# Kernel optimization log

Measured on AMD Instinct MI355X. Metric: run time of the kernel, lower is better.

The kernel has to match this reference:

```python
import jax, jax.numpy as jnp
import numpy as np

N_HEADS = 16

def setup_inputs() -> dict:
    key = jax.random.key(0)
    ks = jax.random.split(key, 7)
    B, S, D = 2, 2048, 1024
    sc = 1.0 / np.sqrt(D)
    return {
        "x": jax.random.normal(ks[0], (B, S, D), dtype=jnp.float32),
        "Wq": jax.random.normal(ks[1], (D, D), dtype=jnp.float32) * sc,
        "bq": jax.random.normal(ks[2], (D,), dtype=jnp.float32) * 0.02,
        "Wk": jax.random.normal(ks[3], (D, D), dtype=jnp.float32) * sc,
        "bk": jax.random.normal(ks[4], (D,), dtype=jnp.float32) * 0.02,
        "Wv": jax.random.normal(ks[5], (D, D), dtype=jnp.float32) * sc,
        "bv": jax.random.normal(ks[6], (D,), dtype=jnp.float32) * 0.02,
    }

def reference(x, Wq, bq, Wk, bk, Wv, bv):
    B, S, D = x.shape
    H = N_HEADS
    W = D // H  # head width
    # QKV projections (torch Linear: x @ W^T + b); here weights stored as [D_in, D_out]
    q = x @ Wq + bq
    k = x @ Wk + bk
    v = x @ Wv + bv
    # split last dim into heads -> [B, H, S, W]
    q = q.reshape(B, S, H, W).transpose(0, 2, 1, 3)
    k = k.reshape(B, S, H, W).transpose(0, 2, 1, 3)
    v = v.reshape(B, S, H, W).transpose(0, 2, 1, 3)
    # scaled dot-product attention; full [B,H,S,S] scores as in original
    scores = jnp.einsum("bhqw,bhkw->bhqk", q, k) / jnp.sqrt(jnp.asarray(W, x.dtype))
    probs = jax.nn.softmax(scores, axis=-1)  # dropout is identity in eval mode
    h = jnp.einsum("bhqk,bhkw->bhqw", probs, v)
    # merge heads -> [B, S, D]
    return h.transpose(0, 2, 1, 3).reshape(B, S, D)
```

## Files before the change

### kernel.cpp

```cpp
#include <hip/hip_runtime.h>

typedef _Float16 H16;
typedef _Float16 half8 __attribute__((ext_vector_type(8)));
typedef _Float16 half4 __attribute__((ext_vector_type(4)));
typedef float f32x4 __attribute__((ext_vector_type(4)));

constexpr int Bb = 2, S = 2048, D = 1024, NH = 16, HW = 64;
constexpr int M = Bb * S;

constexpr size_t XH_OFF = 0;
constexpr size_t WT_OFF = XH_OFF + (size_t)M * D * 2;
constexpr size_t Q_OFF  = WT_OFF + 3ull * D * D * 2;
constexpr size_t K_OFF  = Q_OFF + (size_t)M * D * 2;
constexpr size_t VT_OFF = K_OFF + (size_t)M * D * 2;

#define GLOAD_LDS16(g, l)                                        \
  __builtin_amdgcn_global_load_lds(                              \
      (const __attribute__((address_space(1))) void*)(g),        \
      (__attribute__((address_space(3))) void*)(l), 16, 0, 0)

__global__ __launch_bounds__(256) void prep(const float* __restrict__ x,
                                            H16* __restrict__ xh,
                                            const float* __restrict__ w0,
                                            const float* __restrict__ w1,
                                            const float* __restrict__ w2,
                                            H16* __restrict__ wt) {
  __shared__ H16 tile[64][65];
  const int z = blockIdx.z;
  const int t = threadIdx.x;
  if (z == 0) {
    const int bid = blockIdx.y * 16 + blockIdx.x;
#pragma unroll
    for (int r = 0; r < 8; ++r) {
      size_t i = ((size_t)(bid * 8 + r) * 256 + t) * 8;
      float4 a = *(const float4*)(x + i);
      float4 b = *(const float4*)(x + i + 4);
      half8 h = {(H16)a.x, (H16)a.y, (H16)a.z, (H16)a.w,
                 (H16)b.x, (H16)b.y, (H16)b.z, (H16)b.w};
      *(half8*)(xh + i) = h;
    }
  } else {
    const float* w = z == 1 ? w0 : z == 2 ? w1 : w2;
    H16* out = wt + (size_t)(z - 1) * D * D;
    int c = t & 63, r4 = t >> 6;
    int bx = blockIdx.x * 64, by = blockIdx.y * 64;
#pragma unroll 4
    for (int it = 0; it < 16; ++it) {
      int row = it * 4 + r4;
      tile[c][row] = (H16)w[(size_t)(by + row) * D + bx + c];
    }
    __syncthreads();
#pragma unroll 4
    for (int it = 0; it < 16; ++it) {
      int row = it * 4 + r4;
      out[(size_t)(bx + row) * D + by + c] = tile[row][c];
    }
  }
}

__global__ __launch_bounds__(256) void qkv_gemm(
    const H16* __restrict__ xh, const H16* __restrict__ wt,
    const float* __restrict__ bq, const float* __restrict__ bk,
    const float* __restrict__ bv, H16* __restrict__ qo, H16* __restrict__ ko,
    H16* __restrict__ vto) {
  __shared__ __align__(16) H16 As[128 * 64];
  __shared__ __align__(16) H16 Bs[128 * 64];
  const int lin = blockIdx.x + blockIdx.y * 8 + blockIdx.z * 256;
  const int wid = (lin & 7) * 96 + (lin >> 3);
  const int z = wid >> 8;
  const int rem = wid & 255;
  const int bm = (rem >> 3) * 128, bn = (rem & 7) * 128;
  const H16* w = wt + (size_t)z * D * D;
  const float* bias = z == 0 ? bq : z == 1 ? bk : bv;
  const int t = threadIdx.x;
  const int wave = t >> 6, lane = t & 63;
  const int g = lane >> 4, c = lane & 15;
  const int wm = (wave >> 1) * 64, wn = (wave & 1) * 64;

  const int sw0 = (g ^ (c & 7)) * 8;
  const int sw1 = ((4 + g) ^ (c & 7)) * 8;

  f32x4 acc[4][4] = {};

  for (int kk = 0; kk < D; kk += 64) {
#pragma unroll
    for (int rnd = 0; rnd < 4; ++rnd) {
      int cid = rnd * 256 + t;
      int row = cid >> 3, j = cid & 7;
      int k0 = (j ^ (row & 7)) * 8;
      GLOAD_LDS16(&xh[(size_t)(bm + row) * D + kk + k0], &As[cid * 8]);
      GLOAD_LDS16(&w[(size_t)(bn + row) * D + kk + k0], &Bs[cid * 8]);
    }
    __syncthreads();
#pragma unroll
    for (int kc = 0; kc < 2; ++kc) {
      const int ro = kc ? sw1 : sw0;
      half8 af[4], bf[4];
#pragma unroll
      for (int i = 0; i < 4; ++i) {
        af[i] = *(const half8*)&As[(wm + i * 16 + c) * 64 + ro];
        bf[i] = *(const half8*)&Bs[(wn + i * 16 + c) * 64 + ro];
      }
#pragma unroll
      for (int i = 0; i < 4; ++i)
#pragma unroll
        for (int j2 = 0; j2 < 4; ++j2)
          acc[i][j2] = __builtin_amdgcn_mfma_f32_16x16x32_f16(af[i], bf[j2],
                                                              acc[i][j2], 0, 0, 0);
    }
    __syncthreads();
  }

#pragma unroll
  for (int i = 0; i < 4; ++i) {
#pragma unroll
    for (int j = 0; j < 4; ++j) {
      int coln = bn + wn + j * 16 + c;
      float bse = bias[coln];
      int h = coln >> 6, wcol = coln & 63;
      if (z == 2) {
        int row0 = bm + wm + i * 16 + g * 4;
        int bbx = row0 >> 11, s0 = row0 & (S - 1);
        half4 v4 = {(H16)(acc[i][j][0] + bse), (H16)(acc[i][j][1] + bse),
                    (H16)(acc[i][j][2] + bse), (H16)(acc[i][j][3] + bse)};
        *(half4*)&vto[((size_t)(bbx * NH + h) * HW + wcol) * S + s0] = v4;
      } else {
#pragma unroll
        for (int r = 0; r < 4; ++r) {
          int row = bm + wm + i * 16 + g * 4 + r;
          float val = acc[i][j][r] + bse;
          int bbx = row >> 11, s = row & (S - 1);
          size_t bh = (size_t)(bbx * NH + h);
          if (z == 0)
            qo[(bh * S + s) * HW + wcol] = (H16)val;
          else
            ko[(bh * S + s) * HW + wcol] = (H16)val;
        }
      }
    }
  }
}

__global__ __launch_bounds__(512, 4) void attn(const H16* __restrict__ q,
                                               const H16* __restrict__ k,
                                               const H16* __restrict__ vt,
                                               float* __restrict__ out) {
  constexpr int NIT = S / 128;
  __shared__ __align__(16) H16 Ks[2][2][64 * 64];
  __shared__ __align__(16) H16 Vs[2][2][64 * 64];
  __shared__ float lx[4][2][16];

  const int id = blockIdx.x;
  const int xcd = id & 7, slot = id >> 3;
  const int bh = xcd * 4 + (slot >> 4);
  const int qt = slot & 15;

  const int t = threadIdx.x, wave = t >> 6, lane = t & 63;
  const int kg = wave >> 2, w4 = wave & 3;
  const int g = lane >> 4, c = lane & 15;
  const int q0 = qt * 128 + w4 * 32;
  const H16* qp = q + ((size_t)bh * S + q0) * HW;
  const H16* kp = k + ((size_t)bh * S + kg * (S / 2)) * HW;
  const H16* vp = vt + (size_t)bh * HW * S + kg * (S / 2);

  const int tt = t & 255;
  const int sq = tt >> 3, sj = tt & 7;
  const int kkey = ((sq >> 2) & 3) * 8 + ((sq >> 4) & 1) * 4 + (sq & 3);
  const int scol = (sj ^ (sq & 7)) * 8;
  const H16* kga = kp + (size_t)kkey * HW + scol;
  const H16* kgb = kp + (size_t)(32 + kkey) * HW + scol;
  const H16* vga = vp + (size_t)sq * S + scol;
  const H16* vgb = vp + (size_t)(sq + 32) * S + scol;

#define STAGE(bufi, nck)                                                  \
  {                                                                       \
    GLOAD_LDS16(kga + (size_t)(nck) * HW, &Ks[bufi][kg][tt * 8]);         \
    GLOAD_LDS16(kgb + (size_t)(nck) * HW, &Ks[bufi][kg][2048 + tt * 8]);  \
    GLOAD_LDS16(vga + (nck), &Vs[bufi][kg][tt * 8]);                      \
    GLOAD_LDS16(vgb + (nck), &Vs[bufi][kg][2048 + tt * 8]);               \
  }

  const H16 scq = (H16)(0.125f * 1.44269504088896f);
  half8 qb[2][2];
#pragma unroll
  for (int qg = 0; qg < 2; ++qg) {
    qb[qg][0] = *(const half8*)&qp[(qg * 16 + c) * HW + g * 8];
    qb[qg][1] = *(const half8*)&qp[(qg * 16 + c) * HW + 32 + g * 8];
#pragma unroll
    for (int e = 0; e < 8; ++e) {
      qb[qg][0][e] *= scq;
      qb[qg][1][e] *= scq;
    }
  }

  f32x4 o[4][2] = {};
  float l[2] = {0.f, 0.f};

  const int sw0 = (g ^ (c & 7)) * 8;
  const int sw1 = ((4 + g) ^ (c & 7)) * 8;

  STAGE(0, 0);
  int buf = 0;
  for (int it = 0; it < NIT; ++it) {
    __syncthreads();
    if (it + 1 < NIT) STAGE(buf ^ 1, (it + 1) * 64);

    const H16* ks = Ks[buf][kg];
    const H16* vs = Vs[buf][kg];

    f32x4 st[4][2];
#pragma unroll
    for (int kt = 0; kt < 4; ++kt) {
      const H16* kr = &ks[(kt * 16 + c) * 64];
      half8 ka0 = *(const half8*)&kr[sw0];
      half8 ka1 = *(const half8*)&kr[sw1];
#pragma unroll
      for (int qg = 0; qg < 2; ++qg) {
        f32x4 z = {};
        st[kt][qg] =
            __builtin_amdgcn_mfma_f32_16x16x32_f16(ka0, qb[qg][0], z, 0, 0, 0);
        st[kt][qg] = __builtin_amdgcn_mfma_f32_16x16x32_f16(ka1, qb[qg][1],
                                                            st[kt][qg], 0, 0, 0);
      }
    }

    half8 pb[2][2];
#pragma unroll
    for (int qg = 0; qg < 2; ++qg) {
#pragma unroll
      for (int kt = 0; kt < 4; ++kt) {
        float p0 = __builtin_amdgcn_exp2f(st[kt][qg][0]);
        float p1 = __builtin_amdgcn_exp2f(st[kt][qg][1]);
        float p2 = __builtin_amdgcn_exp2f(st[kt][qg][2]);
        float p3 = __builtin_amdgcn_exp2f(st[kt][qg][3]);
        l[qg] += (p0 + p1) + (p2 + p3);
        pb[qg][kt >> 1][(kt & 1) * 4 + 0] = (H16)p0;
        pb[qg][kt >> 1][(kt & 1) * 4 + 1] = (H16)p1;
        pb[qg][kt >> 1][(kt & 1) * 4 + 2] = (H16)p2;
        pb[qg][kt >> 1][(kt & 1) * 4 + 3] = (H16)p3;
      }
    }

#pragma unroll
    for (int wt = 0; wt < 4; ++wt) {
      const H16* vr = &vs[(wt * 16 + c) * 64];
      half8 va0 = *(const half8*)&vr[sw0];
      half8 va1 = *(const half8*)&vr[sw1];
#pragma unroll
      for (int qg = 0; qg < 2; ++qg) {
        o[wt][qg] = __builtin_amdgcn_mfma_f32_16x16x32_f16(va0, pb[qg][0],
                                                           o[wt][qg], 0, 0, 0);
        o[wt][qg] = __builtin_amdgcn_mfma_f32_16x16x32_f16(va1, pb[qg][1],
                                                           o[wt][qg], 0, 0, 0);
      }
    }
    buf ^= 1;
  }
#undef STAGE

#pragma unroll
  for (int qg = 0; qg < 2; ++qg) {
    l[qg] += __shfl_xor(l[qg], 16, 64);
    l[qg] += __shfl_xor(l[qg], 32, 64);
  }

  __syncthreads();

  float* pex = (float*)Ks;
  if (kg == 1) {
    float* dst = pex + w4 * 2048;
#pragma unroll
    for (int wt = 0; wt < 4; ++wt)
#pragma unroll
      for (int qg = 0; qg < 2; ++qg)
        *(f32x4*)&dst[(wt * 2 + qg) * 256 + lane * 4] = o[wt][qg];
    if (g == 0) {
      lx[w4][0][c] = l[0];
      lx[w4][1][c] = l[1];
    }
  }
  __syncthreads();
  if (kg == 0) {
    const float* src = pex + w4 * 2048;
    const int bbx = bh >> 4, h = bh & 15;
#pragma unroll
    for (int qg = 0; qg < 2; ++qg) {
      const float inv = 1.0f / (l[qg] + lx[w4][qg][c]);
      float* orow = out + ((size_t)bbx * S + q0 + qg * 16 + c) * D + h * HW;
#pragma unroll
      for (int wt = 0; wt < 4; ++wt) {
        f32x4 po = *(const f32x4*)&src[(wt * 2 + qg) * 256 + lane * 4];
        float4 v4 = {(o[wt][qg][0] + po[0]) * inv, (o[wt][qg][1] + po[1]) * inv,
                     (o[wt][qg][2] + po[2]) * inv, (o[wt][qg][3] + po[3]) * inv};
        *(float4*)&orow[wt * 16 + g * 4] = v4;
      }
    }
  }
}

extern "C" void kernel_launch(void* const* d_in, const int* in_sizes, int n_in,
                              void* d_out, int out_size, void* d_ws,
                              size_t ws_size, hipStream_t stream) {
  const float* x = (const float*)d_in[0];
  const float* Wq = (const float*)d_in[1];
  const float* bq = (const float*)d_in[2];
  const float* Wk = (const float*)d_in[3];
  const float* bk = (const float*)d_in[4];
  const float* Wv = (const float*)d_in[5];
  const float* bv = (const float*)d_in[6];
  float* out = (float*)d_out;
  char* ws = (char*)d_ws;
  H16* xh = (H16*)(ws + XH_OFF);
  H16* wt = (H16*)(ws + WT_OFF);
  H16* qw = (H16*)(ws + Q_OFF);
  H16* kw = (H16*)(ws + K_OFF);
  H16* vtw = (H16*)(ws + VT_OFF);

  prep<<<dim3(16, 16, 4), 256, 0, stream>>>(x, xh, Wq, Wk, Wv, wt);
  qkv_gemm<<<dim3(8, 32, 3), 256, 0, stream>>>(xh, wt, bq, bk, bv, qw, kw, vtw);
  attn<<<dim3(512), 512, 0, stream>>>(qw, kw, vtw, out);
}
```

Baseline: 166.5 us.

## Double-buffer QKV GEMM LDS tiles and raise wave priority around MFMA blocks

The QKV projection GEMM now keeps two LDS buffers for the A and B tiles. It issues the global-to-LDS loads for the next k-slice before computing on the current one, which removes the trailing barrier and overlaps memory latency with MFMA work. s_setprio(1)/(0) brackets are also added around the MFMA clusters in both the GEMM and the attention kernel, to favour waves that are issuing matrix ops. The cost is doubled LDS use in the GEMM (64KB), which may reduce occupancy.

```diff
diff --git a/kernel.cpp b/kernel.cpp
--- a/kernel.cpp
+++ b/kernel.cpp
@@ -63,8 +63,8 @@
     const float* __restrict__ bq, const float* __restrict__ bk,
     const float* __restrict__ bv, H16* __restrict__ qo, H16* __restrict__ ko,
     H16* __restrict__ vto) {
-  __shared__ __align__(16) H16 As[128 * 64];
-  __shared__ __align__(16) H16 Bs[128 * 64];
+  __shared__ __align__(16) H16 As[2][128 * 64];
+  __shared__ __align__(16) H16 Bs[2][128 * 64];
   const int lin = blockIdx.x + blockIdx.y * 8 + blockIdx.z * 256;
   const int wid = (lin & 7) * 96 + (lin >> 3);
   const int z = wid >> 8;
@@ -77,39 +77,52 @@
   const int g = lane >> 4, c = lane & 15;
   const int wm = (wave >> 1) * 64, wn = (wave & 1) * 64;
 
+  const int srow = t >> 3, sj = t & 7;
+  const int sk0 = (sj ^ (srow & 7)) * 8;
+
+#define QSTAGE(bufi, kkk)                                                   \
+  {                                                                         \
+    _Pragma("unroll") for (int rnd = 0; rnd < 4; ++rnd) {                   \
+      int row = rnd * 32 + srow;                                            \
+      int cid = rnd * 256 + t;                                              \
+      GLOAD_LDS16(&xh[(size_t)(bm + row) * D + (kkk) + sk0],                \
+                  &As[bufi][cid * 8]);                                      \
+      GLOAD_LDS16(&w[(size_t)(bn + row) * D + (kkk) + sk0],                 \
+                  &Bs[bufi][cid * 8]);                                      \
+    }                                                                       \
+  }
+
   const int sw0 = (g ^ (c & 7)) * 8;
   const int sw1 = ((4 + g) ^ (c & 7)) * 8;
 
   f32x4 acc[4][4] = {};
 
+  QSTAGE(0, 0);
+  int buf = 0;
   for (int kk = 0; kk < D; kk += 64) {
-#pragma unroll
-    for (int rnd = 0; rnd < 4; ++rnd) {
-      int cid = rnd * 256 + t;
-      int row = cid >> 3, j = cid & 7;
-      int k0 = (j ^ (row & 7)) * 8;
-      GLOAD_LDS16(&xh[(size_t)(bm + row) * D + kk + k0], &As[cid * 8]);
-      GLOAD_LDS16(&w[(size_t)(bn + row) * D + kk + k0], &Bs[cid * 8]);
-    }
     __syncthreads();
+    if (kk + 64 < D) QSTAGE(buf ^ 1, kk + 64);
 #pragma unroll
     for (int kc = 0; kc < 2; ++kc) {
       const int ro = kc ? sw1 : sw0;
       half8 af[4], bf[4];
 #pragma unroll
       for (int i = 0; i < 4; ++i) {
-        af[i] = *(const half8*)&As[(wm + i * 16 + c) * 64 + ro];
-        bf[i] = *(const half8*)&Bs[(wn + i * 16 + c) * 64 + ro];
-      }
+        af[i] = *(const half8*)&As[buf][(wm + i * 16 + c) * 64 + ro];
+        bf[i] = *(const half8*)&Bs[buf][(wn + i * 16 + c) * 64 + ro];
+      }
+      __builtin_amdgcn_s_setprio(1);
 #pragma unroll
       for (int i = 0; i < 4; ++i)
 #pragma unroll
         for (int j2 = 0; j2 < 4; ++j2)
           acc[i][j2] = __builtin_amdgcn_mfma_f32_16x16x32_f16(af[i], bf[j2],
                                                               acc[i][j2], 0, 0, 0);
-    }
-    __syncthreads();
-  }
+      __builtin_amdgcn_s_setprio(0);
+    }
+    buf ^= 1;
+  }
+#undef QSTAGE
 
 #pragma unroll
   for (int i = 0; i < 4; ++i) {
@@ -214,6 +227,7 @@
       const H16* kr = &ks[(kt * 16 + c) * 64];
       half8 ka0 = *(const half8*)&kr[sw0];
       half8 ka1 = *(const half8*)&kr[sw1];
+      __builtin_amdgcn_s_setprio(1);
 #pragma unroll
       for (int qg = 0; qg < 2; ++qg) {
         f32x4 z = {};
@@ -222,6 +236,7 @@
         st[kt][qg] = __builtin_amdgcn_mfma_f32_16x16x32_f16(ka1, qb[qg][1],
                                                             st[kt][qg], 0, 0, 0);
       }
+      __builtin_amdgcn_s_setprio(0);
     }
 
     half8 pb[2][2];
@@ -246,6 +261,7 @@
       const H16* vr = &vs[(wt * 16 + c) * 64];
       half8 va0 = *(const half8*)&vr[sw0];
       half8 va1 = *(const half8*)&vr[sw1];
+      __builtin_amdgcn_s_setprio(1);
 #pragma unroll
       for (int qg = 0; qg < 2; ++qg) {
         o[wt][qg] = __builtin_amdgcn_mfma_f32_16x16x32_f16(va0, pb[qg][0],
@@ -253,6 +269,7 @@
         o[wt][qg] = __builtin_amdgcn_mfma_f32_16x16x32_f16(va1, pb[qg][1],
                                                            o[wt][qg], 0, 0, 0);
       }
+      __builtin_amdgcn_s_setprio(0);
     }
     buf ^= 1;
   }
```

Result: no change. 169.0 us (+1.5%).

## Load K/V fragments directly from global memory instead of LDS staging

Applied to the files above, without the earlier changes.

Removes the double-buffered LDS staging of K and V tiles (global_load_lds plus __syncthreads per iteration). Each lane now reads its MFMA operand fragments straight from global memory, relying on L1/L2 since the four query waves share the same keys. It also interleaves the QK MFMAs with exp2 per key tile and adds s_setprio around MFMA groups. This drops barriers and LDS traffic but adds redundant global loads, with no software prefetch to hide their latency.

```diff
diff --git a/kernel.cpp b/kernel.cpp
--- a/kernel.cpp
+++ b/kernel.cpp
@@ -146,8 +146,7 @@
                                                const H16* __restrict__ vt,
                                                float* __restrict__ out) {
   constexpr int NIT = S / 128;
-  __shared__ __align__(16) H16 Ks[2][2][64 * 64];
-  __shared__ __align__(16) H16 Vs[2][2][64 * 64];
+  __shared__ float pex[4][2048];
   __shared__ float lx[4][2][16];
 
   const int id = blockIdx.x;
@@ -163,23 +162,6 @@
   const H16* kp = k + ((size_t)bh * S + kg * (S / 2)) * HW;
   const H16* vp = vt + (size_t)bh * HW * S + kg * (S / 2);
 
-  const int tt = t & 255;
-  const int sq = tt >> 3, sj = tt & 7;
-  const int kkey = ((sq >> 2) & 3) * 8 + ((sq >> 4) & 1) * 4 + (sq & 3);
-  const int scol = (sj ^ (sq & 7)) * 8;
-  const H16* kga = kp + (size_t)kkey * HW + scol;
-  const H16* kgb = kp + (size_t)(32 + kkey) * HW + scol;
-  const H16* vga = vp + (size_t)sq * S + scol;
-  const H16* vgb = vp + (size_t)(sq + 32) * S + scol;
-
-#define STAGE(bufi, nck)                                                  \
-  {                                                                       \
-    GLOAD_LDS16(kga + (size_t)(nck) * HW, &Ks[bufi][kg][tt * 8]);         \
-    GLOAD_LDS16(kgb + (size_t)(nck) * HW, &Ks[bufi][kg][2048 + tt * 8]);  \
-    GLOAD_LDS16(vga + (nck), &Vs[bufi][kg][tt * 8]);                      \
-    GLOAD_LDS16(vgb + (nck), &Vs[bufi][kg][2048 + tt * 8]);               \
-  }
-
   const H16 scq = (H16)(0.125f * 1.44269504088896f);
   half8 qb[2][2];
 #pragma unroll
@@ -193,46 +175,44 @@
     }
   }
 
+  const H16* klane = kp + (size_t)(8 * (c >> 2) + (c & 3)) * HW + g * 8;
+  const H16* vlane = vp + (size_t)c * S + g * 8;
+
   f32x4 o[4][2] = {};
   float l[2] = {0.f, 0.f};
 
-  const int sw0 = (g ^ (c & 7)) * 8;
-  const int sw1 = ((4 + g) ^ (c & 7)) * 8;
-
-  STAGE(0, 0);
-  int buf = 0;
   for (int it = 0; it < NIT; ++it) {
-    __syncthreads();
-    if (it + 1 < NIT) STAGE(buf ^ 1, (it + 1) * 64);
-
-    const H16* ks = Ks[buf][kg];
-    const H16* vs = Vs[buf][kg];
-
-    f32x4 st[4][2];
+    const int kofs = it * 64 * HW;
+    const int vofs = it * 64;
+
+    half8 kf[4][2];
 #pragma unroll
     for (int kt = 0; kt < 4; ++kt) {
-      const H16* kr = &ks[(kt * 16 + c) * 64];
-      half8 ka0 = *(const half8*)&kr[sw0];
-      half8 ka1 = *(const half8*)&kr[sw1];
+      const int ko = kofs + (32 * (kt >> 1) + 4 * (kt & 1)) * HW;
+      kf[kt][0] = *(const half8*)(klane + ko);
+      kf[kt][1] = *(const half8*)(klane + ko + 32);
+    }
+
+    half8 pb[2][2];
+#pragma unroll
+    for (int kt = 0; kt < 4; ++kt) {
+      f32x4 st[2];
+      __builtin_amdgcn_s_setprio(1);
 #pragma unroll
       for (int qg = 0; qg < 2; ++qg) {
         f32x4 z = {};
-        st[kt][qg] =
-            __builtin_amdgcn_mfma_f32_16x16x32_f16(ka0, qb[qg][0], z, 0, 0, 0);
-        st[kt][qg] = __builtin_amdgcn_mfma_f32_16x16x32_f16(ka1, qb[qg][1],
-                                                            st[kt][qg], 0, 0, 0);
-      }
-    }
-
-    half8 pb[2][2];
-#pragma unroll
-    for (int qg = 0; qg < 2; ++qg) {
-#pragma unroll
-      for (int kt = 0; kt < 4; ++kt) {
-        float p0 = __builtin_amdgcn_exp2f(st[kt][qg][0]);
-        float p1 = __builtin_amdgcn_exp2f(st[kt][qg][1]);
-        float p2 = __builtin_amdgcn_exp2f(st[kt][qg][2]);
-        float p3 = __builtin_amdgcn_exp2f(st[kt][qg][3]);
+        st[qg] = __builtin_amdgcn_mfma_f32_16x16x32_f16(kf[kt][0], qb[qg][0],
+                                                        z, 0, 0, 0);
+        st[qg] = __builtin_amdgcn_mfma_f32_16x16x32_f16(kf[kt][1], qb[qg][1],
+                                                        st[qg], 0, 0, 0);
+      }
+      __builtin_amdgcn_s_setprio(0);
+#pragma unroll
+      for (int qg = 0; qg < 2; ++qg) {
+        float p0 = __builtin_amdgcn_exp2f(st[qg][0]);
+        float p1 = __builtin_amdgcn_exp2f(st[qg][1]);
+        float p2 = __builtin_amdgcn_exp2f(st[qg][2]);
+        float p3 = __builtin_amdgcn_exp2f(st[qg][3]);
         l[qg] += (p0 + p1) + (p2 + p3);
         pb[qg][kt >> 1][(kt & 1) * 4 + 0] = (H16)p0;
         pb[qg][kt >> 1][(kt & 1) * 4 + 1] = (H16)p1;
@@ -243,20 +223,19 @@
 
 #pragma unroll
     for (int wt = 0; wt < 4; ++wt) {
-      const H16* vr = &vs[(wt * 16 + c) * 64];
-      half8 va0 = *(const half8*)&vr[sw0];
-      half8 va1 = *(const half8*)&vr[sw1];
+      half8 v0 = *(const half8*)(vlane + (size_t)wt * 16 * S + vofs);
+      half8 v1 = *(const half8*)(vlane + (size_t)wt * 16 * S + vofs + 32);
+      __builtin_amdgcn_s_setprio(1);
 #pragma unroll
       for (int qg = 0; qg < 2; ++qg) {
-        o[wt][qg] = __builtin_amdgcn_mfma_f32_16x16x32_f16(va0, pb[qg][0],
+        o[wt][qg] = __builtin_amdgcn_mfma_f32_16x16x32_f16(v0, pb[qg][0],
                                                            o[wt][qg], 0, 0, 0);
-        o[wt][qg] = __builtin_amdgcn_mfma_f32_16x16x32_f16(va1, pb[qg][1],
+        o[wt][qg] = __builtin_amdgcn_mfma_f32_16x16x32_f16(v1, pb[qg][1],
                                                            o[wt][qg], 0, 0, 0);
       }
-    }
-    buf ^= 1;
-  }
-#undef STAGE
+      __builtin_amdgcn_s_setprio(0);
+    }
+  }
 
 #pragma unroll
   for (int qg = 0; qg < 2; ++qg) {
@@ -264,11 +243,8 @@
     l[qg] += __shfl_xor(l[qg], 32, 64);
   }
 
-  __syncthreads();
-
-  float* pex = (float*)Ks;
   if (kg == 1) {
-    float* dst = pex + w4 * 2048;
+    float* dst = pex[w4];
 #pragma unroll
     for (int wt = 0; wt < 4; ++wt)
 #pragma unroll
@@ -281,7 +257,7 @@
   }
   __syncthreads();
   if (kg == 0) {
-    const float* src = pex + w4 * 2048;
+    const float* src = pex[w4];
     const int bbx = bh >> 4, h = bh & 15;
 #pragma unroll
     for (int qg = 0; qg < 2; ++qg) {
```

New measurement: 243.8 us. +46.4%, slower.
